# Kernel optimization log

Measured on AMD Instinct MI355X. Metric: run time of the kernel, lower is better.

The kernel has to match this reference:

```python
import jax, jax.numpy as jnp
import numpy as np

N_HEADS = 16
N_KV = 8
HEAD_DIM = 128
HID = 2048
GROUPS = N_HEADS // N_KV
THETA = 10000.0


def _rope_cos_sin(position_ids, dtype):
    # position_ids: [1, S] int
    inv_freq = 1.0 / (THETA ** (jnp.arange(0, HEAD_DIM, 2, dtype=jnp.float32) / HEAD_DIM))
    freqs = position_ids.astype(jnp.float32)[:, :, None] * inv_freq[None, None, :]  # [1,S,hd/2]
    emb = jnp.concatenate([freqs, freqs], axis=-1)  # [1,S,hd]
    return jnp.cos(emb).astype(dtype)[:, None, :, :], jnp.sin(emb).astype(dtype)[:, None, :, :]


def _rotate_half(x):
    x1, x2 = x[..., : HEAD_DIM // 2], x[..., HEAD_DIM // 2 :]
    return jnp.concatenate([-x2, x1], axis=-1)


def setup_inputs() -> dict:
    key = jax.random.key(0)
    ks = jax.random.split(key, 8)
    B, S = 2, 2048
    hidden_states = jax.random.normal(ks[0], (B, S, HID), jnp.float32)
    Wq = jax.random.normal(ks[1], (HID, N_HEADS * HEAD_DIM), jnp.float32) * 0.02
    Wk = jax.random.normal(ks[2], (HID, N_KV * HEAD_DIM), jnp.float32) * 0.02
    Wv = jax.random.normal(ks[3], (HID, N_KV * HEAD_DIM), jnp.float32) * 0.02
    Wo = jax.random.normal(ks[4], (HID, HID), jnp.float32) * 0.02
    gate = jnp.zeros((1, N_HEADS, 1, 1), jnp.float32)
    memory_in = jax.random.normal(ks[5], (B, N_KV, HEAD_DIM, HEAD_DIM), jnp.float32)
    norm_in = jax.random.uniform(ks[6], (B, N_KV, 1, HEAD_DIM), jnp.float32)
    position_ids = jnp.arange(S, dtype=jnp.int32)[None, :]
    return {"hidden_states": hidden_states, "Wq": Wq, "Wk": Wk, "Wv": Wv, "Wo": Wo,
            "gate": gate, "memory_in": memory_in, "norm_in": norm_in,
            "position_ids": position_ids}


def reference(hidden_states, Wq, Wk, Wv, Wo, gate, memory_in, norm_in, position_ids):
    B, S, _ = hidden_states.shape
    # projections -> [B, H, S, hd]
    q = jnp.einsum('bsh,ho->bso', hidden_states, Wq).reshape(B, S, N_HEADS, HEAD_DIM).transpose(0, 2, 1, 3)
    k = jnp.einsum('bsh,ho->bso', hidden_states, Wk).reshape(B, S, N_KV, HEAD_DIM).transpose(0, 2, 1, 3)
    v = jnp.einsum('bsh,ho->bso', hidden_states, Wv).reshape(B, S, N_KV, HEAD_DIM).transpose(0, 2, 1, 3)

    # ---- compressive memory retrieval (pre-RoPE q, as in original) ----
    sigma_q = jax.nn.elu(q) + 1.0  # [B, nH, S, hd]
    mem_tiled = jnp.tile(memory_in, (1, GROUPS, 1, 1))          # torch .repeat tiles
    norm_tiled = jnp.tile(norm_in, (1, GROUPS, 1, 1))            # [B, nH, 1, hd]
    memory_output = jnp.einsum('bhsd,bhde->bhse', sigma_q, mem_tiled)
    norm_bcast = jnp.einsum('bhsd,bhd->bhs', sigma_q, norm_tiled[:, :, 0, :])[..., None]
    memory_output = memory_output / norm_bcast

    # ---- memory update (pre-RoPE k, v) ----
    sigma_k = jax.nn.elu(k) + 1.0  # [B, nKV, S, hd]
    updated_memory = memory_in + jnp.einsum('bhsd,bhse->bhde', sigma_k, v)
    updated_norm = norm_in + jnp.sum(sigma_k, axis=2, keepdims=True)

    # ---- RoPE ----
    cos, sin = _rope_cos_sin(position_ids, q.dtype)
    q = q * cos + _rotate_half(q) * sin
    k = k * cos + _rotate_half(k) * sin

    # ---- repeat_kv (interleave, groups) ----
    k = jnp.repeat(k, GROUPS, axis=1)
    v = jnp.repeat(v, GROUPS, axis=1)

    # ---- causal SDPA ----
    scale = 1.0 / np.sqrt(HEAD_DIM)
    scores = jnp.einsum('bhqd,bhkd->bhqk', q, k) * scale
    causal = jnp.tril(jnp.ones((S, S), dtype=bool))
    scores = jnp.where(causal[None, None], scores, jnp.finfo(scores.dtype).min)
    probs = jax.nn.softmax(scores, axis=-1)
    attn = jnp.einsum('bhqk,bhkd->bhqd', probs, v)

    # ---- gated combination + output projection ----
    g = jax.nn.sigmoid(gate)
    combined = g * memory_output + (1.0 - g) * attn  # [B, nH, S, hd]
    combined = combined.transpose(0, 2, 1, 3).reshape(B, S, HID)
    final_output = jnp.einsum('bsh,ho->bso', combined, Wo)
    return final_output, updated_memory, updated_norm
```

## Files before the change

### kernel.cpp

```cpp
#include <hip/hip_runtime.h>

#define BATCH 2
#define SEQ   2048
#define HID   2048
#define NH    16
#define NKV   8
#define HD    128
#define M_ROWS (BATCH * SEQ)
#define QKV_N  4096

typedef __attribute__((ext_vector_type(8))) __bf16 bf16x8;
typedef __attribute__((ext_vector_type(4))) float  f32x4;

static __device__ __forceinline__ f32x4 mfma16(bf16x8 a, bf16x8 b, f32x4 c) {
    return __builtin_amdgcn_mfma_f32_16x16x32_bf16(a, b, c, 0, 0, 0);
}
static __device__ __forceinline__ float sigma_f(float x) {
    return x > 0.f ? x + 1.f : __expf(x);
}
static __device__ __forceinline__ void gload16(const __bf16* g, __bf16* l) {
    __builtin_amdgcn_global_load_lds(
        (const __attribute__((address_space(1))) void*)g,
        (__attribute__((address_space(3))) void*)l, 16, 0, 0);
}

#define OFF_QKV  0ull
#define OFF_SQ   67108864ull
#define OFF_QR   83886080ull
#define OFF_KR   100663296ull
#define OFF_VT   109051904ull
#define OFF_ND   117440512ull
#define OFF_CB   117702656ull
#define OFF_PART 134479872ull
#define OFF_BND  142868480ull
#define OFF_MAXP 143130624ull
#define OFF_NPART 143134720ull
#define NSPLIT 8

__global__ __launch_bounds__(256) void pre_k(const float* __restrict__ hidden,
                                             const float* __restrict__ Wq,
                                             const float* __restrict__ Wk,
                                             const float* __restrict__ Wv,
                                             __bf16* __restrict__ hb,
                                             __bf16* __restrict__ qkvT)
{
    __shared__ __bf16 T[64][72];
    const int bid = blockIdx.x;
    const int t = threadIdx.x;
    if (bid < 4096) {
        const size_t i = ((size_t)bid * 256 + t) * 8;
        const float4 v0 = *reinterpret_cast<const float4*>(hidden + i);
        const float4 v1 = *reinterpret_cast<const float4*>(hidden + i + 4);
        bf16x8 o;
        o[0]=(__bf16)v0.x; o[1]=(__bf16)v0.y; o[2]=(__bf16)v0.z; o[3]=(__bf16)v0.w;
        o[4]=(__bf16)v1.x; o[5]=(__bf16)v1.y; o[6]=(__bf16)v1.z; o[7]=(__bf16)v1.w;
        *reinterpret_cast<bf16x8*>(hb + i) = o;
        return;
    }
    int tb = bid - 4096;
    const float* W; __bf16* Bt; int N;
    if (tb < 1024)      { W = Wq; Bt = qkvT;                         N = 2048; }
    else if (tb < 1536) { W = Wk; Bt = qkvT + (size_t)2048 * HID;    N = 1024; tb -= 1024; }
    else                { W = Wv; Bt = qkvT + (size_t)3072 * HID;    N = 1024; tb -= 1536; }
    const int k0 = (tb & 31) * 64, n0 = (tb >> 5) * 64;
    #pragma unroll
    for (int i = 0; i < 4; ++i) {
        const int idx = t + i * 256;
        const int r = idx >> 4, c4 = (idx & 15) * 4;
        const float4 v = *reinterpret_cast<const float4*>(&W[(size_t)(k0 + r) * N + n0 + c4]);
        T[c4 + 0][r] = (__bf16)v.x; T[c4 + 1][r] = (__bf16)v.y;
        T[c4 + 2][r] = (__bf16)v.z; T[c4 + 3][r] = (__bf16)v.w;
    }
    __syncthreads();
    #pragma unroll
    for (int i = 0; i < 2; ++i) {
        const int idx = t + i * 256;
        const int rr = idx >> 3, cc = (idx & 7) * 8;
        *reinterpret_cast<bf16x8*>(&Bt[(size_t)(n0 + rr) * HID + k0 + cc]) =
            *reinterpret_cast<bf16x8*>(&T[rr][cc]);
    }
}

__global__ __launch_bounds__(256) void tr_k(const float* __restrict__ W,
                                            __bf16* __restrict__ Bt, int K, int N)
{
    __shared__ __bf16 T[64][72];
    const int k0 = blockIdx.x * 64, n0 = blockIdx.y * 64;
    const int t = threadIdx.x;
    #pragma unroll
    for (int i = 0; i < 4; ++i) {
        const int idx = t + i * 256;
        const int r = idx >> 4, c4 = (idx & 15) * 4;
        const float4 v = *reinterpret_cast<const float4*>(&W[(size_t)(k0 + r) * N + n0 + c4]);
        T[c4 + 0][r] = (__bf16)v.x; T[c4 + 1][r] = (__bf16)v.y;
        T[c4 + 2][r] = (__bf16)v.z; T[c4 + 3][r] = (__bf16)v.w;
    }
    __syncthreads();
    #pragma unroll
    for (int i = 0; i < 2; ++i) {
        const int idx = t + i * 256;
        const int rr = idx >> 3, cc = (idx & 7) * 8;
        *reinterpret_cast<bf16x8*>(&Bt[(size_t)(n0 + rr) * K + k0 + cc]) =
            *reinterpret_cast<bf16x8*>(&T[rr][cc]);
    }
}

__global__ __launch_bounds__(512, 2) void gemm8_k(const __bf16* __restrict__ A,
                                                  const __bf16* __restrict__ Bt,
                                                  float* __restrict__ C,
                                                  int N, int K)
{
    __shared__ __align__(16) __bf16 smem[65536];
    const int tid = threadIdx.x, wave = tid >> 6, lane = tid & 63;
    const int l15 = lane & 15, l4 = lane >> 4;
    const int wr = wave >> 2, wc = wave & 3;

    const int nwg = gridDim.x;
    const int swz = (blockIdx.x & 7) * (nwg >> 3) + (blockIdx.x >> 3);
    const int NBN = N >> 8;
    const int bm = swz / NBN, bn = swz - bm * NBN;
    const int m0 = bm << 8, n0 = bn << 8;

    const int NKT = K >> 6;

    const int srow   = tid >> 2;
    const int schunk = (tid & 3) ^ ((tid >> 3) & 3);
    const int sdst   = wave * 512;

    const int achunk = l4 ^ ((l15 >> 1) & 3);
    const int aoff = (wr * 128 + l15) * 32 + achunk * 8;
    const int boff = (wc * 64  + l15) * 32 + achunk * 8;

    f32x4 acc[2][4][4] = {};
    bf16x8 af[4], bfr[4];

#define STAGE_SLAB(gb, r0, koff, slabptr) do {                                   \
        const __bf16* _g = (gb) + (size_t)((r0) + srow) * K + (koff) + schunk * 8; \
        gload16(_g,                    (slabptr) + sdst);                        \
        gload16(_g + (size_t)128 * K,  (slabptr) + sdst + 4096);                 \
    } while (0)

    STAGE_SLAB(A,  m0, 0,  smem);
    STAGE_SLAB(Bt, n0, 0,  smem + 16384);
    STAGE_SLAB(A,  m0, 32, smem + 8192);
    STAGE_SLAB(Bt, n0, 32, smem + 24576);
    STAGE_SLAB(A,  m0, 64, smem + 32768);
    STAGE_SLAB(Bt, n0, 64, smem + 32768 + 16384);
    asm volatile("s_waitcnt vmcnt(4)" ::: "memory");
    __builtin_amdgcn_s_barrier();

    #pragma unroll 1
    for (int T = 0; T < NKT; ++T) {
        __bf16* bufc = smem + (T & 1) * 32768;
        __bf16* bufn = smem + ((T & 1) ^ 1) * 32768;
        const int kt1 = (T + 1) * 64, kt2 = (T + 2) * 64;

        {
            const __bf16* As = bufc;
            const __bf16* Bs = bufc + 16384;
            #pragma unroll
            for (int f = 0; f < 4; ++f)  af[f]  = *reinterpret_cast<const bf16x8*>(As + aoff + f * 512);
            #pragma unroll
            for (int nf = 0; nf < 4; ++nf) bfr[nf] = *reinterpret_cast<const bf16x8*>(Bs + boff + nf * 512);
            if (T + 1 < NKT) STAGE_SLAB(A, m0, kt1 + 32, bufn + 8192);
            __builtin_amdgcn_s_barrier();
            __builtin_amdgcn_s_setprio(1);
            #pragma unroll
            for (int f = 0; f < 4; ++f)
                #pragma unroll
                for (int nf = 0; nf < 4; ++nf)
                    acc[0][f][nf] = mfma16(af[f], bfr[nf], acc[0][f][nf]);
            __builtin_amdgcn_s_setprio(0);
            __builtin_amdgcn_s_barrier();
        }
        {
            const __bf16* As = bufc;
            #pragma unroll
            for (int f = 0; f < 4; ++f)  af[f] = *reinterpret_cast<const bf16x8*>(As + aoff + 2048 + f * 512);
            if (T + 1 < NKT) STAGE_SLAB(Bt, n0, kt1 + 32, bufn + 24576);
            __builtin_amdgcn_s_barrier();
            __builtin_amdgcn_s_setprio(1);
            #pragma unroll
            for (int f = 0; f < 4; ++f)
                #pragma unroll
                for (int nf = 0; nf < 4; ++nf)
                    acc[1][f][nf] = mfma16(af[f], bfr[nf], acc[1][f][nf]);
            __builtin_amdgcn_s_setprio(0);
            __builtin_amdgcn_s_barrier();
        }
        {
            const __bf16* As = bufc + 8192;
            const __bf16* Bs = bufc + 24576;
            #pragma unroll
            for (int f = 0; f < 4; ++f)  af[f]  = *reinterpret_cast<const bf16x8*>(As + aoff + f * 512);
            #pragma unroll
            for (int nf = 0; nf < 4; ++nf) bfr[nf] = *reinterpret_cast<const bf16x8*>(Bs + boff + nf * 512);
            if (T + 2 < NKT) STAGE_SLAB(A, m0, kt2, bufc);
            __builtin_amdgcn_s_barrier();
            __builtin_amdgcn_s_setprio(1);
            #pragma unroll
            for (int f = 0; f < 4; ++f)
                #pragma unroll
                for (int nf = 0; nf < 4; ++nf)
                    acc[0][f][nf] = mfma16(af[f], bfr[nf], acc[0][f][nf]);
            __builtin_amdgcn_s_setprio(0);
            __builtin_amdgcn_s_barrier();
        }
        {
            const __bf16* As = bufc + 8192;
            #pragma unroll
            for (int f = 0; f < 4; ++f)  af[f] = *reinterpret_cast<const bf16x8*>(As + aoff + 2048 + f * 512);
            if (T + 2 < NKT) STAGE_SLAB(Bt, n0, kt2, bufc + 16384);
            __builtin_amdgcn_s_barrier();
            __builtin_amdgcn_s_setprio(1);
            #pragma unroll
            for (int f = 0; f < 4; ++f)
                #pragma unroll
                for (int nf = 0; nf < 4; ++nf)
                    acc[1][f][nf] = mfma16(af[f], bfr[nf], acc[1][f][nf]);
            __builtin_amdgcn_s_setprio(0);
            if (T < NKT - 2) asm volatile("s_waitcnt vmcnt(4)" ::: "memory");
            else             asm volatile("s_waitcnt vmcnt(0)" ::: "memory");
            __builtin_amdgcn_s_barrier();
        }
    }
#undef STAGE_SLAB

    #pragma unroll
    for (int mh = 0; mh < 2; ++mh)
        #pragma unroll
        for (int f = 0; f < 4; ++f)
            #pragma unroll
            for (int nf = 0; nf < 4; ++nf)
                #pragma unroll
                for (int r = 0; r < 4; ++r) {
                    const int row = m0 + wr * 128 + mh * 64 + f * 16 + l4 * 4 + r;
                    const int col = n0 + wc * 64 + nf * 16 + l15;
                    C[(size_t)row * N + col] = acc[mh][f][nf][r];
                }
}

__global__ __launch_bounds__(512, 2) void gemm8n_k(const __bf16* __restrict__ A,
                                                   const __bf16* __restrict__ Bt,
                                                   float* __restrict__ C,
                                                   int N, int K)
{
    __shared__ __align__(16) __bf16 smem[49152];
    const int tid = threadIdx.x, wave = tid >> 6, lane = tid & 63;
    const int l15 = lane & 15, l4 = lane >> 4;
    const int wr = wave >> 2, wc = wave & 3;

    const int nwg = gridDim.x;
    const int swz = (blockIdx.x & 7) * (nwg >> 3) + (blockIdx.x >> 3);
    const int NBN = N >> 8;
    const int bm = swz / NBN, bn = swz - bm * NBN;
    const int m0 = bm << 7, n0 = bn << 8;

    const int NKT = K >> 6;

    const int srow   = tid >> 2;
    const int schunk = (tid & 3) ^ ((tid >> 3) & 3);
    const int sdst   = wave * 512;

    const int achunk = l4 ^ ((l15 >> 1) & 3);
    const int aoff = (wr * 64 + l15) * 32 + achunk * 8;
    const int boff = (wc * 64 + l15) * 32 + achunk * 8;

    f32x4 acc[4][4] = {};
    bf16x8 af[4], bfr[4];

#define STAGE_A(koff, dstp) do {                                                  \
        gload16(A + (size_t)(m0 + srow) * K + (koff) + schunk * 8, (dstp) + sdst); \
    } while (0)
#define STAGE_B(koff, dstp) do {                                                  \
        const __bf16* _g = Bt + (size_t)(n0 + srow) * K + (koff) + schunk * 8;    \
        gload16(_g,                   (dstp) + sdst);                             \
        gload16(_g + (size_t)128 * K, (dstp) + sdst + 4096);                      \
    } while (0)

    STAGE_A(0,  smem);
    STAGE_B(0,  smem + 8192);
    STAGE_A(32, smem + 4096);
    STAGE_B(32, smem + 16384);
    STAGE_A(64, smem + 24576);
    STAGE_B(64, smem + 24576 + 8192);
    asm volatile("s_waitcnt vmcnt(3)" ::: "memory");
    __builtin_amdgcn_s_barrier();

    #pragma unroll 1
    for (int T = 0; T < NKT; ++T) {
        __bf16* bufc = smem + (T & 1) * 24576;
        __bf16* bufn = smem + ((T & 1) ^ 1) * 24576;
        const int kt1 = (T + 1) * 64, kt2 = (T + 2) * 64;

        {
            #pragma unroll
            for (int f = 0; f < 4; ++f)  af[f]  = *reinterpret_cast<const bf16x8*>(bufc + aoff + f * 512);
            #pragma unroll
            for (int nf = 0; nf < 4; ++nf) bfr[nf] = *reinterpret_cast<const bf16x8*>(bufc + 8192 + boff + nf * 512);
            if (T + 1 < NKT) { STAGE_A(kt1 + 32, bufn + 4096); STAGE_B(kt1 + 32, bufn + 16384); }
            __builtin_amdgcn_s_barrier();
            __builtin_amdgcn_s_setprio(1);
            #pragma unroll
            for (int f = 0; f < 4; ++f)
                #pragma unroll
                for (int nf = 0; nf < 4; ++nf)
                    acc[f][nf] = mfma16(af[f], bfr[nf], acc[f][nf]);
            __builtin_amdgcn_s_setprio(0);
            __builtin_amdgcn_s_barrier();
        }
        {
            #pragma unroll
            for (int f = 0; f < 4; ++f)  af[f]  = *reinterpret_cast<const bf16x8*>(bufc + 4096 + aoff + f * 512);
            #pragma unroll
            for (int nf = 0; nf < 4; ++nf) bfr[nf] = *reinterpret_cast<const bf16x8*>(bufc + 16384 + boff + nf * 512);
            if (T + 2 < NKT) { STAGE_A(kt2, bufc); STAGE_B(kt2, bufc + 8192); }
            __builtin_amdgcn_s_barrier();
            __builtin_amdgcn_s_setprio(1);
            #pragma unroll
            for (int f = 0; f < 4; ++f)
                #pragma unroll
                for (int nf = 0; nf < 4; ++nf)
                    acc[f][nf] = mfma16(af[f], bfr[nf], acc[f][nf]);
            __builtin_amdgcn_s_setprio(0);
            if (T < NKT - 2) asm volatile("s_waitcnt vmcnt(3)" ::: "memory");
            else             asm volatile("s_waitcnt vmcnt(0)" ::: "memory");
            __builtin_amdgcn_s_barrier();
        }
    }
#undef STAGE_A
#undef STAGE_B

    #pragma unroll
    for (int f = 0; f < 4; ++f)
        #pragma unroll
        for (int nf = 0; nf < 4; ++nf)
            #pragma unroll
            for (int r = 0; r < 4; ++r) {
                const int row = m0 + wr * 64 + f * 16 + l4 * 4 + r;
                const int col = n0 + wc * 64 + nf * 16 + l15;
                C[(size_t)row * N + col] = acc[f][nf][r];
            }
}

__global__ __launch_bounds__(256) void prep_k(const float* __restrict__ qkv,
                                              const float* __restrict__ norm_in,
                                              const int* __restrict__ pos_ids,
                                              __bf16* __restrict__ sq, __bf16* __restrict__ qr,
                                              __bf16* __restrict__ kr, __bf16* __restrict__ vt,
                                              float* __restrict__ nd, float* __restrict__ bnd,
                                              float* __restrict__ maxp)
{
    const int sc = blockIdx.x, kvh = blockIdx.y, b = blockIdx.z;
    const int s0 = sc * 32, t = threadIdx.x;
    const float scale = 0.08838834764831845f;
    const float s2 = scale * scale;
    const float NEG_LN_TH = -0.14391156831212787f;
    __shared__ float krn[32];

    {
        const int row = t >> 2;
        const int head = row >> 5, sl = row & 31;
        const int hq = kvh * 2 + head, nh = hq & 7;
        const int dq = (t & 3) * 16;
        const int pos = pos_ids[s0 + sl];
        const float* qp = qkv + (size_t)(b * SEQ + s0 + sl) * QKV_N + hq * 128;
        const float* np = norm_in + (b * NKV + nh) * 128;

        float x0[16], x1[16];
        #pragma unroll
        for (int i = 0; i < 16; i += 4) {
            *reinterpret_cast<float4*>(&x0[i]) = *reinterpret_cast<const float4*>(qp + dq + i);
            *reinterpret_cast<float4*>(&x1[i]) = *reinterpret_cast<const float4*>(qp + dq + 64 + i);
        }
        float nds = 0.f, qns = 0.f;
        bf16x8 sqv0[2], sqv1[2], qrv0[2], qrv1[2];
        #pragma unroll
        for (int i = 0; i < 16; ++i) {
            const int j = dq + i;
            float c, sn;
            __sincosf((float)pos * __expf((float)j * NEG_LN_TH), &sn, &c);
            qrv0[i >> 3][i & 7] = (__bf16)((x0[i] * c - x1[i] * sn) * scale);
            qrv1[i >> 3][i & 7] = (__bf16)((x1[i] * c + x0[i] * sn) * scale);
            const float sg0 = sigma_f(x0[i]), sg1 = sigma_f(x1[i]);
            sqv0[i >> 3][i & 7] = (__bf16)sg0;
            sqv1[i >> 3][i & 7] = (__bf16)sg1;
            nds += sg0 * np[j] + sg1 * np[j + 64];
            qns += (x0[i] * x0[i] + x1[i] * x1[i]) * s2;
        }
        __bf16* sqp = sq + ((size_t)(b * NH + hq) * SEQ + s0 + sl) * 128;
        __bf16* qrp = qr + ((size_t)(b * NH + hq) * SEQ + s0 + sl) * 128;
        *reinterpret_cast<bf16x8*>(sqp + dq)      = sqv0[0];
        *reinterpret_cast<bf16x8*>(sqp + dq + 8)  = sqv0[1];
        *reinterpret_cast<bf16x8*>(sqp + dq + 64) = sqv1[0];
        *reinterpret_cast<bf16x8*>(sqp + dq + 72) = sqv1[1];
        *reinterpret_cast<bf16x8*>(qrp + dq)      = qrv0[0];
        *reinterpret_cast<bf16x8*>(qrp + dq + 8)  = qrv0[1];
        *reinterpret_cast<bf16x8*>(qrp + dq + 64) = qrv1[0];
        *reinterpret_cast<bf16x8*>(qrp + dq + 72) = qrv1[1];

        nds += __shfl_xor(nds, 1); nds += __shfl_xor(nds, 2);
        qns += __shfl_xor(qns, 1); qns += __shfl_xor(qns, 2);
        if ((t & 3) == 0) {
            nd [(size_t)(b * NH + hq) * SEQ + s0 + sl] = nds;
            bnd[(size_t)(b * NH + hq) * SEQ + s0 + sl] = qns;
        }
    }

    if (t < 128) {
        const int sl = t >> 2;
        const int dq = (t & 3) * 16;
        const int pos = pos_ids[s0 + sl];
        const float* kp = qkv + (size_t)(b * SEQ + s0 + sl) * QKV_N + 2048 + kvh * 128;
        float x0[16], x1[16];
        #pragma unroll
        for (int i = 0; i < 16; i += 4) {
            *reinterpret_cast<float4*>(&x0[i]) = *reinterpret_cast<const float4*>(kp + dq + i);
            *reinterpret_cast<float4*>(&x1[i]) = *reinterpret_cast<const float4*>(kp + dq + 64 + i);
        }
        bf16x8 kv0[2], kv1[2];
        float kns = 0.f;
        #pragma unroll
        for (int i = 0; i < 16; ++i) {
            const int j = dq + i;
            float c, sn;
            __sincosf((float)pos * __expf((float)j * NEG_LN_TH), &sn, &c);
            kv0[i >> 3][i & 7] = (__bf16)(x0[i] * c - x1[i] * sn);
            kv1[i >> 3][i & 7] = (__bf16)(x1[i] * c + x0[i] * sn);
            kns += x0[i] * x0[i] + x1[i] * x1[i];
        }
        __bf16* krp = kr + ((size_t)(b * NKV + kvh) * SEQ + s0 + sl) * 128;
        *reinterpret_cast<bf16x8*>(krp + dq)      = kv0[0];
        *reinterpret_cast<bf16x8*>(krp + dq + 8)  = kv0[1];
        *reinterpret_cast<bf16x8*>(krp + dq + 64) = kv1[0];
        *reinterpret_cast<bf16x8*>(krp + dq + 72) = kv1[1];
        kns += __shfl_xor(kns, 1); kns += __shfl_xor(kns, 2);
        if ((t & 3) == 0) krn[sl] = kns;
    }

    __shared__ float vl[128][33];
    {
        const int sl = t >> 3, dch = (t & 7) * 16;
        const float* vp = qkv + (size_t)(b * SEQ + s0 + sl) * QKV_N + 3072 + kvh * 128 + dch;
        float xv[16];
        #pragma unroll
        for (int i = 0; i < 16; i += 4)
            *reinterpret_cast<float4*>(&xv[i]) = *reinterpret_cast<const float4*>(vp + i);
        #pragma unroll
        for (int i = 0; i < 16; ++i) vl[dch + i][sl] = xv[i];
    }
    __syncthreads();
    if (t == 0) {
        float mx = 0.f;
        #pragma unroll
        for (int i = 0; i < 32; ++i) mx = fmaxf(mx, krn[i]);
        maxp[((b * NKV + kvh) << 6) + sc] = mx;
    }
    {
        const int d = t >> 1, sh = (t & 1) * 16;
        bf16x8 o0, o1;
        #pragma unroll
        for (int j = 0; j < 8; ++j) o0[j] = (__bf16)vl[d][sh + j];
        #pragma unroll
        for (int j = 0; j < 8; ++j) o1[j] = (__bf16)vl[d][sh + 8 + j];
        __bf16* vp = vt + ((size_t)((b * NKV + kvh) * 128 + d)) * SEQ + s0 + sh;
        *reinterpret_cast<bf16x8*>(vp)     = o0;
        *reinterpret_cast<bf16x8*>(vp + 8) = o1;
    }
}

__global__ __launch_bounds__(256) void memout_k(const __bf16* __restrict__ sq,
                                                const float* __restrict__ mem_in,
                                                const float* __restrict__ nd,
                                                const float* __restrict__ gate,
                                                __bf16* __restrict__ cb)
{
    __shared__ __align__(16) __bf16 mt[128][136];
    const int tid = threadIdx.x;
    const int h = blockIdx.y, b = blockIdx.z;
    const int s0 = blockIdx.x * 64;

    const float* mem = mem_in + (size_t)(b * NKV + (h & 7)) * 16384;
    for (int i = tid; i < 16384; i += 256) {
        int dd = i >> 7, e = i & 127;
        mt[e][dd] = (__bf16)mem[i];
    }
    __syncthreads();

    const int wave = tid >> 6, lane = tid & 63, l15 = lane & 15, l4 = lane >> 4;
    f32x4 acc[8] = {};
    const __bf16* sqb = sq + ((size_t)(b * NH + h) * SEQ + s0 + wave * 16 + l15) * 128;
    #pragma unroll
    for (int kb = 0; kb < 4; ++kb) {
        bf16x8 a = *reinterpret_cast<const bf16x8*>(sqb + kb * 32 + l4 * 8);
        #pragma unroll
        for (int nc = 0; nc < 8; ++nc) {
            bf16x8 bb = *reinterpret_cast<bf16x8*>(&mt[nc * 16 + l15][kb * 32 + l4 * 8]);
            acc[nc] = mfma16(a, bb, acc[nc]);
        }
    }
    float g = 1.f / (1.f + __expf(-gate[h]));
    #pragma unroll
    for (int r = 0; r < 4; ++r) {
        int srow = s0 + wave * 16 + l4 * 4 + r;
        float scl = g / nd[(size_t)(b * NH + h) * SEQ + srow];
        __bf16* cbp = cb + (size_t)(b * SEQ + srow) * HID + h * 128;
        #pragma unroll
        for (int nc = 0; nc < 8; ++nc)
            cbp[nc * 16 + l15] = (__bf16)(acc[nc][r] * scl);
    }
}

__global__ __launch_bounds__(256) void memupd_k(const float* __restrict__ qkv,
                                                float* __restrict__ part,
                                                float* __restrict__ npart)
{
    const int sp = blockIdx.x, h = blockIdx.y, b = blockIdx.z;
    const int tid = threadIdx.x;
    const int tx = tid & 15, ty = tid >> 4;
    __shared__ __align__(16) float sk[8][128];
    __shared__ __align__(16) float sv[8][128];
    float acc[8][8] = {};
    float nacc = 0.f;

    const int s0 = sp * (SEQ / NSPLIT);
    for (int so = 0; so < SEQ / NSPLIT; so += 8) {
        for (int i = tid; i < 8 * 128; i += 256) {
            int rr = i >> 7, dd = i & 127;
            const float* rowp = qkv + (size_t)(b * SEQ + s0 + so + rr) * QKV_N;
            sk[rr][dd] = sigma_f(rowp[2048 + h * 128 + dd]);
            sv[rr][dd] = rowp[3072 + h * 128 + dd];
        }
        __syncthreads();
        if (tid < 128) {
            #pragma unroll
            for (int rr = 0; rr < 8; ++rr) nacc += sk[rr][tid];
        }
        #pragma unroll
        for (int rr = 0; rr < 8; ++rr) {
            float4 k0 = *reinterpret_cast<float4*>(&sk[rr][tx * 8]);
            float4 k1 = *reinterpret_cast<float4*>(&sk[rr][tx * 8 + 4]);
            float4 v0 = *reinterpret_cast<float4*>(&sv[rr][ty * 8]);
            float4 v1 = *reinterpret_cast<float4*>(&sv[rr][ty * 8 + 4]);
            float kreg[8] = {k0.x,k0.y,k0.z,k0.w,k1.x,k1.y,k1.z,k1.w};
            float vreg[8] = {v0.x,v0.y,v0.z,v0.w,v1.x,v1.y,v1.z,v1.w};
            #pragma unroll
            for (int i = 0; i < 8; ++i)
                #pragma unroll
                for (int j2 = 0; j2 < 8; ++j2)
                    acc[i][j2] += kreg[i] * vreg[j2];
        }
        __syncthreads();
    }
    float* pb = part + ((size_t)sp * (BATCH * NKV) + b * NKV + h) * 16384;
    #pragma unroll
    for (int i = 0; i < 8; ++i)
        #pragma unroll
        for (int j2 = 0; j2 < 8; ++j2)
            pb[(tx * 8 + i) * 128 + ty * 8 + j2] = acc[i][j2];
    if (tid < 128)
        npart[((size_t)sp * (BATCH * NKV) + b * NKV + h) * 128 + tid] = nacc;
}

__global__ __launch_bounds__(256) void memrednorm_k(const float* __restrict__ part,
                                                    const float* __restrict__ mem_in,
                                                    float* __restrict__ out_mem,
                                                    const float* __restrict__ npart,
                                                    const float* __restrict__ norm_in,
                                                    float* __restrict__ out_norm)
{
    const int bid = blockIdx.x;
    if (bid < 1024) {
        const size_t i = (size_t)bid * 256 + threadIdx.x;
        float a = mem_in[i];
        #pragma unroll
        for (int sp = 0; sp < NSPLIT; ++sp) a += part[(size_t)sp * 262144 + i];
        out_mem[i] = a;
    } else if (threadIdx.x < 128) {
        const int bh = bid - 1024, d = threadIdx.x;
        float a = norm_in[bh * 128 + d];
        #pragma unroll
        for (int sp = 0; sp < NSPLIT; ++sp)
            a += npart[((size_t)sp * (BATCH * NKV) + bh) * 128 + d];
        out_norm[bh * 128 + d] = a;
    }
}

__global__ __launch_bounds__(256, 2) void attn_k(const __bf16* __restrict__ qr,
                                                 const __bf16* __restrict__ kr,
                                                 const __bf16* __restrict__ vt,
                                                 const float* __restrict__ gate,
                                                 const float* __restrict__ bnd,
                                                 const float* __restrict__ maxp,
                                                 __bf16* __restrict__ cb)
{
    __shared__ __align__(16) char smem[81920];
    char* ksB = smem;
    char* vsB = smem + 32768;
    char* pB  = smem + 65536;
    float*  red  = (float*)smem;
    float*  lred = (float*)(smem + 65536);

    const int tid = threadIdx.x, wave = tid >> 6, lane = tid & 63;
    const int l15 = lane & 15, l4 = lane >> 4;
    const int e3 = l15 & 7, e2 = e3 >> 2;
    const int ksub = wave >> 1;
    const int wq   = wave & 1;

    const int n   = blockIdx.x + 16 * (blockIdx.y + 16 * blockIdx.z);
    const int xcd = n & 7, i64 = n >> 3;
    const int grp = xcd * 2 + (i64 >> 5);
    const int within = i64 & 31;
    const int b   = grp >> 3;
    const int kvh = grp & 7;
    const int h   = kvh * 2 + (within >> 4);
    const int x   = within & 15;

    const __bf16* kbase = kr + (size_t)(b * NKV + kvh) * SEQ * 128;
    const __bf16* vbase = vt + (size_t)(b * NKV + kvh) * 128 * SEQ;
    const float* bbase  = bnd + (size_t)(b * NH + h) * SEQ;

    const float g  = 1.f / (1.f + __expf(-gate[h]));
    const float gi = 1.f - g;
    float kn2 = 0.f;
    const float* mp = maxp + (b * NKV + kvh) * 64;
    #pragma unroll
    for (int i = 0; i < 64; i += 4) {
        const float4 v = *reinterpret_cast<const float4*>(mp + i);
        kn2 = fmaxf(kn2, fmaxf(fmaxf(v.x, v.y), fmaxf(v.z, v.w)));
    }
    const float knmax = sqrtf(kn2);

    bf16x8 ones;
    #pragma unroll
    for (int j = 0; j < 8; ++j) ones[j] = (__bf16)1.0f;

    const int srow = wave * 32 + l4;
    const int chA  = (lane & 15) ^ l4;
    const char* KG0 = (const char*)kbase + srow * 256 + chA * 16;
    const char* KG1 = (const char*)kbase + srow * 256 + ((chA ^ 4) * 16);
    const char* VG0 = (const char*)vbase + srow * 4096 + chA * 16;
    const char* VG1 = (const char*)vbase + srow * 4096 + ((chA ^ 4) * 16);
    __bf16* kdst = (__bf16*)(ksB + wave * 8192);
    __bf16* vdst = (__bf16*)(vsB + wave * 8192);

    const int t16 = (l4 ^ (e3 & 3)) * 16;
    const int KBe = l15 * 256 + ksub * 16384 + t16 + e2 * 64;
    const int KBo = l15 * 256 + ksub * 16384 + t16 + (1 ^ e2) * 64;
    const int VB0 = l15 * 256 + t16 + e2 * 64 + ksub * 128;
    const int VB1 = l15 * 256 + t16 + (1 ^ e2) * 64 + ksub * 128;
    const int PWb = wave * 4096 + (l15 & 7) * 2;
    const int PR  = wave * 4096 + l15 * 128 + ((l4 ^ e3) * 16);

#define ISSUE_K(ktrow) do {                                                      \
        const int _ko = (ktrow) * 256;                                           \
        _Pragma("unroll")                                                        \
        for (int _j = 0; _j < 8; ++_j)                                           \
            gload16((const __bf16*)(((_j & 1) ? KG1 : KG0) + _ko + _j * 1024),   \
                    kdst + _j * 512);                                            \
    } while (0)
#define ISSUE_V(ktrow) do {                                                      \
        const int _vo = (ktrow) * 2;                                             \
        _Pragma("unroll")                                                        \
        for (int _j = 0; _j < 8; ++_j)                                           \
            gload16((const __bf16*)(((_j & 1) ? VG1 : VG0) + _vo + _j * 16384),  \
                    vdst + _j * 512);                                            \
    } while (0)

    #pragma unroll 1
    for (int tile = 0; tile < 2; ++tile) {
        const int q0 = (tile == 0 ? x : 31 - x) * 64;
        const int qw = q0 + wq * 32;
        const int NT = (q0 >> 6) + 1;
        const int NI = (NT + 1) >> 1;

        bf16x8 af[2][4];
        float m_r[2][4];
        #pragma unroll
        for (int m = 0; m < 2; ++m) {
            const __bf16* qb = qr + ((size_t)(b * NH + h) * SEQ + qw + m * 16 + l15) * 128;
            #pragma unroll
            for (int kb = 0; kb < 4; ++kb)
                af[m][kb] = *reinterpret_cast<const bf16x8*>(qb + kb * 32 + l4 * 8);
            #pragma unroll
            for (int r = 0; r < 4; ++r)
                m_r[m][r] = sqrtf(bbase[qw + m * 16 + l4 * 4 + r]) * knmax + 1.0f;
        }

        f32x4 o0[8] = {}, o1[8] = {};
        f32x4 lc0 = {}, lc1 = {};

        ISSUE_K(0);
        ISSUE_V(0);
        asm volatile("s_waitcnt vmcnt(8)" ::: "memory");
        __builtin_amdgcn_sched_barrier(0);
        __builtin_amdgcn_s_barrier();

        #pragma unroll 1
        for (int it = 0; it < NI; ++it) {
            const int s = 2 * it + ksub;
            const bool act  = (s < NT);
            const bool more = (it + 1 < NI);

            f32x4 s0[4] = {}, s1[4] = {};
            if (act) {
                __builtin_amdgcn_s_setprio(1);
                #pragma unroll
                for (int kb = 0; kb < 4; ++kb) {
                    const int kbb = ((kb & 1) ? KBo : KBe) + (kb >> 1) * 128;
                    #pragma unroll
                    for (int sub = 0; sub < 4; ++sub) {
                        bf16x8 bb = *reinterpret_cast<const bf16x8*>(ksB + kbb + sub * 4096);
                        s0[sub] = mfma16(af[0][kb], bb, s0[sub]);
                        s1[sub] = mfma16(af[1][kb], bb, s1[sub]);
                    }
                }
                __builtin_amdgcn_s_setprio(0);
            }
            __builtin_amdgcn_sched_barrier(0);
            __builtin_amdgcn_s_barrier();

            if (more) ISSUE_K((it + 1) * 128);

            if (act) {
                #pragma unroll
                for (int r = 0; r < 4; ++r) {
                    const int q0r = qw + l4 * 4 + r;
                    const int q1r = q0r + 16;
                    const int p0r = l4 * 4 + r;
                    const int rw0 = PWb + p0r * 128;
                    #pragma unroll
                    for (int sub = 0; sub < 4; ++sub) {
                        const int key = s * 64 + sub * 16 + l15;
                        float p0 = __expf(s0[sub][r] - m_r[0][r]);
                        float p1 = __expf(s1[sub][r] - m_r[1][r]);
                        p0 = (key <= q0r) ? p0 : 0.f;
                        p1 = (key <= q1r) ? p1 : 0.f;
                        const int cc = (sub * 2 + (l15 >> 3)) ^ (p0r & 7);
                        *(__bf16*)(pB + rw0 + cc * 16)        = (__bf16)p0;
                        *(__bf16*)(pB + rw0 + cc * 16 + 2048) = (__bf16)p1;
                    }
                }
            }
            if (more) asm volatile("s_waitcnt vmcnt(8)" ::: "memory");
            else      asm volatile("s_waitcnt vmcnt(0)" ::: "memory");
            __builtin_amdgcn_sched_barrier(0);
            __builtin_amdgcn_s_barrier();

            if (act) {
                bf16x8 a00 = *reinterpret_cast<const bf16x8*>(pB + PR);
                bf16x8 a01 = *reinterpret_cast<const bf16x8*>(pB + (PR ^ 64));
                bf16x8 a10 = *reinterpret_cast<const bf16x8*>(pB + PR + 2048);
                bf16x8 a11 = *reinterpret_cast<const bf16x8*>(pB + (PR ^ 64) + 2048);
                __builtin_amdgcn_s_setprio(1);
                lc0 = mfma16(a00, ones, lc0); lc0 = mfma16(a01, ones, lc0);
                lc1 = mfma16(a10, ones, lc1); lc1 = mfma16(a11, ones, lc1);
                #pragma unroll
                for (int nc = 0; nc < 8; ++nc) {
                    bf16x8 b0 = *reinterpret_cast<const bf16x8*>(vsB + VB0 + nc * 4096);
                    bf16x8 b1 = *reinterpret_cast<const bf16x8*>(vsB + VB1 + nc * 4096);
                    o0[nc] = mfma16(a00, b0, o0[nc]); o0[nc] = mfma16(a01, b1, o0[nc]);
                    o1[nc] = mfma16(a10, b0, o1[nc]); o1[nc] = mfma16(a11, b1, o1[nc]);
                }
                __builtin_amdgcn_s_setprio(0);
            }
            __builtin_amdgcn_sched_barrier(0);
            __builtin_amdgcn_s_barrier();

            if (more) {
                ISSUE_V((it + 1) * 128);
                asm volatile("s_waitcnt vmcnt(8)" ::: "memory");
            } else {
                asm volatile("s_waitcnt vmcnt(0)" ::: "memory");
            }
            __builtin_amdgcn_sched_barrier(0);
            __builtin_amdgcn_s_barrier();
        }

        if (wave >= 2) {
            float* rb = red + (wave - 2) * 4224;
            #pragma unroll
            for (int nc = 0; nc < 8; ++nc)
                #pragma unroll
                for (int r = 0; r < 4; ++r) {
                    rb[(l4 * 4 + r) * 132 + nc * 16 + l15]        = o0[nc][r];
                    rb[(16 + l4 * 4 + r) * 132 + nc * 16 + l15]   = o1[nc][r];
                }
            if (l15 == 0) {
                float* lb = lred + (wave - 2) * 32;
                #pragma unroll
                for (int r = 0; r < 4; ++r) {
                    lb[l4 * 4 + r]      = lc0[r];
                    lb[16 + l4 * 4 + r] = lc1[r];
                }
            }
        }
        __syncthreads();
        if (wave < 2) {
            float* rb = red + wave * 4224;
            const float* lb = lred + wave * 32;
            #pragma unroll
            for (int r = 0; r < 4; ++r) {
                const int qrow = qw + l4 * 4 + r;
                const float i0 = gi / (lc0[r] + lb[l4 * 4 + r]);
                const float i1 = gi / (lc1[r] + lb[16 + l4 * 4 + r]);
                __bf16* c0 = cb + (size_t)(b * SEQ + qrow) * HID + h * 128;
                __bf16* c1 = cb + (size_t)(b * SEQ + qrow + 16) * HID + h * 128;
                #pragma unroll
                for (int nc = 0; nc < 8; ++nc) {
                    const int dd = nc * 16 + l15;
                    const float v0 = o0[nc][r] + rb[(l4 * 4 + r) * 132 + dd];
                    const float v1 = o1[nc][r] + rb[(16 + l4 * 4 + r) * 132 + dd];
                    c0[dd] = (__bf16)((float)c0[dd] + v0 * i0);
                    c1[dd] = (__bf16)((float)c1[dd] + v1 * i1);
                }
            }
        }
        __syncthreads();
    }
#undef ISSUE_K
#undef ISSUE_V
}

extern "C" void kernel_launch(void* const* d_in, const int* in_sizes, int n_in,
                              void* d_out, int out_size, void* d_ws, size_t ws_size,
                              hipStream_t stream)
{
    const float* hidden  = (const float*)d_in[0];
    const float* Wq      = (const float*)d_in[1];
    const float* Wk      = (const float*)d_in[2];
    const float* Wv      = (const float*)d_in[3];
    const float* Wo      = (const float*)d_in[4];
    const float* gate    = (const float*)d_in[5];
    const float* mem_in  = (const float*)d_in[6];
    const float* norm_in = (const float*)d_in[7];
    const int*   pos     = (const int*)d_in[8];

    float* out_final = (float*)d_out;
    float* out_mem   = out_final + (size_t)BATCH * SEQ * HID;
    float* out_norm  = out_mem + (size_t)BATCH * NKV * 128 * 128;

    char* ws = (char*)d_ws;
    float*  qkv  = (float*)(ws + OFF_QKV);
    __bf16* sq   = (__bf16*)(ws + OFF_SQ);
    __bf16* qrb  = (__bf16*)(ws + OFF_QR);
    __bf16* krb  = (__bf16*)(ws + OFF_KR);
    __bf16* vtb  = (__bf16*)(ws + OFF_VT);
    float*  nd   = (float*)(ws + OFF_ND);
    __bf16* cb   = (__bf16*)(ws + OFF_CB);
    float*  part = (float*)(ws + OFF_PART);
    float*  bnd  = (float*)(ws + OFF_BND);
    float*  maxp = (float*)(ws + OFF_MAXP);
    float*  npart = (float*)(ws + OFF_NPART);
    __bf16* hb   = (__bf16*)(ws + OFF_SQ);
    __bf16* qkvT = (__bf16*)(ws + OFF_QR);
    __bf16* woT  = (__bf16*)(ws + OFF_PART);

    pre_k<<<6144, 256, 0, stream>>>(hidden, Wq, Wk, Wv, hb, qkvT);

    gemm8_k<<<(M_ROWS / 256) * (QKV_N / 256), 512, 0, stream>>>(hb, qkvT, qkv, QKV_N, HID);

    prep_k<<<dim3(SEQ / 32, NKV, BATCH), 256, 0, stream>>>(qkv, norm_in, pos, sq, qrb, krb, vtb,
                                                           nd, bnd, maxp);

    memout_k<<<dim3(SEQ / 64, NH, BATCH), 256, 0, stream>>>(sq, mem_in, nd, gate, cb);

    memupd_k<<<dim3(NSPLIT, NKV, BATCH), 256, 0, stream>>>(qkv, part, npart);
    memrednorm_k<<<1040, 256, 0, stream>>>(part, mem_in, out_mem, npart, norm_in, out_norm);

    tr_k<<<dim3(HID / 64, HID / 64), 256, 0, stream>>>(Wo, woT, HID, HID);

    attn_k<<<dim3(16, NH, BATCH), 256, 0, stream>>>(qrb, krb, vtb, gate, bnd, maxp, cb);

    gemm8n_k<<<(M_ROWS / 128) * (HID / 256), 512, 0, stream>>>(cb, woT, out_final, HID, HID);
}
```

Before: 440.1 us.

## Split memory-update kernel over value halves and change P tile LDS layout

```diff
diff --git a/kernel.cpp b/kernel.cpp
--- a/kernel.cpp
+++ b/kernel.cpp
@@ -515,24 +515,29 @@
                                                 float* __restrict__ part,
                                                 float* __restrict__ npart)
 {
-    const int sp = blockIdx.x, h = blockIdx.y, b = blockIdx.z;
+    const int sp = blockIdx.x, yy = blockIdx.y, b = blockIdx.z;
+    const int h = yy & 7, eh = yy >> 3;
     const int tid = threadIdx.x;
     const int tx = tid & 15, ty = tid >> 4;
     __shared__ __align__(16) float sk[8][128];
-    __shared__ __align__(16) float sv[8][128];
-    float acc[8][8] = {};
+    __shared__ __align__(16) float sv[8][64];
+    float acc[8][4] = {};
     float nacc = 0.f;
 
     const int s0 = sp * (SEQ / NSPLIT);
     for (int so = 0; so < SEQ / NSPLIT; so += 8) {
         for (int i = tid; i < 8 * 128; i += 256) {
             int rr = i >> 7, dd = i & 127;
-            const float* rowp = qkv + (size_t)(b * SEQ + s0 + so + rr) * QKV_N;
-            sk[rr][dd] = sigma_f(rowp[2048 + h * 128 + dd]);
-            sv[rr][dd] = rowp[3072 + h * 128 + dd];
+            sk[rr][dd] = sigma_f(qkv[(size_t)(b * SEQ + s0 + so + rr) * QKV_N + 2048 + h * 128 + dd]);
+        }
+        {
+            const int rr = tid >> 6, ee = tid & 63;
+            const size_t base = (size_t)(b * SEQ + s0 + so) * QKV_N + 3072 + h * 128 + eh * 64 + ee;
+            sv[rr][ee]     = qkv[base + (size_t)rr * QKV_N];
+            sv[rr + 4][ee] = qkv[base + (size_t)(rr + 4) * QKV_N];
         }
         __syncthreads();
-        if (tid < 128) {
+        if (eh == 0 && tid < 128) {
             #pragma unroll
             for (int rr = 0; rr < 8; ++rr) nacc += sk[rr][tid];
         }
@@ -540,25 +545,24 @@
         for (int rr = 0; rr < 8; ++rr) {
             float4 k0 = *reinterpret_cast<float4*>(&sk[rr][tx * 8]);
             float4 k1 = *reinterpret_cast<float4*>(&sk[rr][tx * 8 + 4]);
-            float4 v0 = *reinterpret_cast<float4*>(&sv[rr][ty * 8]);
-            float4 v1 = *reinterpret_cast<float4*>(&sv[rr][ty * 8 + 4]);
+            float4 v0 = *reinterpret_cast<float4*>(&sv[rr][ty * 4]);
             float kreg[8] = {k0.x,k0.y,k0.z,k0.w,k1.x,k1.y,k1.z,k1.w};
-            float vreg[8] = {v0.x,v0.y,v0.z,v0.w,v1.x,v1.y,v1.z,v1.w};
+            float vreg[4] = {v0.x,v0.y,v0.z,v0.w};
             #pragma unroll
             for (int i = 0; i < 8; ++i)
                 #pragma unroll
-                for (int j2 = 0; j2 < 8; ++j2)
+                for (int j2 = 0; j2 < 4; ++j2)
                     acc[i][j2] += kreg[i] * vreg[j2];
         }
         __syncthreads();
     }
     float* pb = part + ((size_t)sp * (BATCH * NKV) + b * NKV + h) * 16384;
     #pragma unroll
-    for (int i = 0; i < 8; ++i)
-        #pragma unroll
-        for (int j2 = 0; j2 < 8; ++j2)
-            pb[(tx * 8 + i) * 128 + ty * 8 + j2] = acc[i][j2];
-    if (tid < 128)
+    for (int i = 0; i < 8; ++i) {
+        float4 o; o.x = acc[i][0]; o.y = acc[i][1]; o.z = acc[i][2]; o.w = acc[i][3];
+        *reinterpret_cast<float4*>(&pb[(tx * 8 + i) * 128 + eh * 64 + ty * 4]) = o;
+    }
+    if (eh == 0 && tid < 128)
         npart[((size_t)sp * (BATCH * NKV) + b * NKV + h) * 128 + tid] = nacc;
 }
 
@@ -649,8 +653,8 @@
     const int KBo = l15 * 256 + ksub * 16384 + t16 + (1 ^ e2) * 64;
     const int VB0 = l15 * 256 + t16 + e2 * 64 + ksub * 128;
     const int VB1 = l15 * 256 + t16 + (1 ^ e2) * 64 + ksub * 128;
-    const int PWb = wave * 4096 + (l15 & 7) * 2;
-    const int PR  = wave * 4096 + l15 * 128 + ((l4 ^ e3) * 16);
+    const int PWw = wave * 4096 + l4 * 512 + l15 * 2;
+    const int PWr = wave * 4096 + l15 * 128 + l4 * 16;
 
 #define ISSUE_K(ktrow) do {                                                      \
         const int _ko = (ktrow) * 256;                                           \
@@ -727,8 +731,6 @@
                 for (int r = 0; r < 4; ++r) {
                     const int q0r = qw + l4 * 4 + r;
                     const int q1r = q0r + 16;
-                    const int p0r = l4 * 4 + r;
-                    const int rw0 = PWb + p0r * 128;
                     #pragma unroll
                     for (int sub = 0; sub < 4; ++sub) {
                         const int key = s * 64 + sub * 16 + l15;
@@ -736,9 +738,8 @@
                         float p1 = __expf(s1[sub][r] - m_r[1][r]);
                         p0 = (key <= q0r) ? p0 : 0.f;
                         p1 = (key <= q1r) ? p1 : 0.f;
-                        const int cc = (sub * 2 + (l15 >> 3)) ^ (p0r & 7);
-                        *(__bf16*)(pB + rw0 + cc * 16)        = (__bf16)p0;
-                        *(__bf16*)(pB + rw0 + cc * 16 + 2048) = (__bf16)p1;
+                        *(__bf16*)(pB + PWw + r * 128 + sub * 32)        = (__bf16)p0;
+                        *(__bf16*)(pB + PWw + 2048 + r * 128 + sub * 32) = (__bf16)p1;
                     }
                 }
             }
@@ -748,10 +749,10 @@
             __builtin_amdgcn_s_barrier();
 
             if (act) {
-                bf16x8 a00 = *reinterpret_cast<const bf16x8*>(pB + PR);
-                bf16x8 a01 = *reinterpret_cast<const bf16x8*>(pB + (PR ^ 64));
-                bf16x8 a10 = *reinterpret_cast<const bf16x8*>(pB + PR + 2048);
-                bf16x8 a11 = *reinterpret_cast<const bf16x8*>(pB + (PR ^ 64) + 2048);
+                bf16x8 a00 = *reinterpret_cast<const bf16x8*>(pB + PWr);
+                bf16x8 a01 = *reinterpret_cast<const bf16x8*>(pB + PWr + 64);
+                bf16x8 a10 = *reinterpret_cast<const bf16x8*>(pB + PWr + 2048);
+                bf16x8 a11 = *reinterpret_cast<const bf16x8*>(pB + PWr + 2048 + 64);
                 __builtin_amdgcn_s_setprio(1);
                 lc0 = mfma16(a00, ones, lc0); lc0 = mfma16(a01, ones, lc0);
                 lc1 = mfma16(a10, ones, lc1); lc1 = mfma16(a11, ones, lc1);
@@ -865,7 +866,7 @@
 
     memout_k<<<dim3(SEQ / 64, NH, BATCH), 256, 0, stream>>>(sq, mem_in, nd, gate, cb);
 
-    memupd_k<<<dim3(NSPLIT, NKV, BATCH), 256, 0, stream>>>(qkv, part, npart);
+    memupd_k<<<dim3(NSPLIT, 16, BATCH), 256, 0, stream>>>(qkv, part, npart);
     memrednorm_k<<<1040, 256, 0, stream>>>(part, mem_in, out_mem, npart, norm_in, out_norm);
 
     tr_k<<<dim3(HID / 64, HID / 64), 256, 0, stream>>>(Wo, woT, HID, HID);
```

Measured after the change: 426.4 us. 3.1% less time.
